# Optimization experiments

Measured on AMD Instinct MI355X. Metric: run time of the kernel, lower is better.

Reference implementation:

```python
import jax, jax.numpy as jnp
import numpy as np

N, E = 50000, 800000
IN_C, HID, HEADS, NUM_CLASSES = 256, 64, 4, 10
LRELU_SLOPE = 0.2
LN_EPS = 1e-5


def setup_inputs() -> dict:
    key = jax.random.key(0)
    ks = jax.random.split(key, 12)
    HC = HEADS * HID
    glorot = lambda k, shp: jax.random.normal(k, shp, jnp.float32) * np.sqrt(2.0 / (shp[0] + shp[-1]))
    return {
        "x": jax.random.normal(ks[0], (N, IN_C), jnp.float32),
        "edge_index": jax.random.randint(ks[1], (2, E), 0, N, jnp.int64),
        "edge_weight": jax.random.uniform(ks[2], (E, 1), jnp.float32),
        "W": glorot(ks[3], (IN_C, HC)),
        "att_src": glorot(ks[4], (1, HEADS, HID)),
        "att_dst": glorot(ks[5], (1, HEADS, HID)),
        "att_edge": glorot(ks[6], (1, HEADS, HID)),
        "W_edge": glorot(ks[7], (1, HC)),
        "bias": jnp.zeros((HC,), jnp.float32),
        "ln_gamma": jnp.ones((HC,), jnp.float32),
        "ln_beta": jnp.zeros((HC,), jnp.float32),
        "fc_W": glorot(ks[8], (HC, NUM_CLASSES)),
        "fc_b": jnp.zeros((NUM_CLASSES,), jnp.float32),
    }


def reference(x, edge_index, edge_weight, W, att_src, att_dst, att_edge,
              W_edge, bias, ln_gamma, ln_beta, fc_W, fc_b):
    n = x.shape[0]
    src, dst = edge_index[0], edge_index[1]

    # GATConv: linear projection -> [N, H, C]
    xh = (x @ W).reshape(n, HEADS, HID)
    a_src = jnp.sum(xh * att_src, axis=-1)  # [N, H]
    a_dst = jnp.sum(xh * att_dst, axis=-1)  # [N, H]

    # edge feature projection (edge_dim=1) -> per-edge attention term
    eh = (edge_weight @ W_edge).reshape(-1, HEADS, HID)  # [E, H, C]
    a_edge = jnp.sum(eh * att_edge, axis=-1)             # [E, H]

    alpha = a_src[src] + a_dst[dst] + a_edge             # [E, H]
    alpha = jax.nn.leaky_relu(alpha, LRELU_SLOPE)

    # segment softmax over incoming edges of each destination node
    amax = jax.ops.segment_max(alpha, dst, num_segments=n)  # [N, H]
    amax = jnp.where(jnp.isfinite(amax), amax, 0.0)
    ex = jnp.exp(alpha - amax[dst])
    esum = jax.ops.segment_sum(ex, dst, num_segments=n)     # [N, H]
    attn = ex / (esum[dst] + 1e-16)                          # [E, H]

    # message = gathered source features weighted by attention; scatter-add
    msg = xh[src] * attn[:, :, None]                          # [E, H, C]
    out = jax.ops.segment_sum(msg, dst, num_segments=n)      # [N, H, C]
    out = out.reshape(n, HEADS * HID) + bias                  # concat heads

    # LayerNorm + ReLU (dropout is identity in eval) + Linear head
    mu = jnp.mean(out, axis=-1, keepdims=True)
    var = jnp.mean(jnp.square(out - mu), axis=-1, keepdims=True)
    out = (out - mu) * jax.lax.rsqrt(var + LN_EPS) * ln_gamma + ln_beta
    out = jax.nn.relu(out)
    return out @ fc_W + fc_b
```

## Files before the change

kernel.cpp:

```cpp
#include <hip/hip_runtime.h>
#include <hip/hip_bf16.h>

static constexpr int HEADS = 4;
static constexpr int HID   = 64;
static constexpr int HC    = 256;
static constexpr int NCLS  = 10;

typedef short    bf16x8 __attribute__((ext_vector_type(8)));
typedef _Float16 f16x8  __attribute__((ext_vector_type(8)));
typedef _Float16 f16x4  __attribute__((ext_vector_type(4)));
typedef float    f32x4  __attribute__((ext_vector_type(4)));

__device__ inline unsigned short f2bf(float f) {
    union { float f; unsigned u; } c; c.f = f;
    unsigned r = (c.u + 0x7fff + ((c.u >> 16) & 1)) >> 16;
    return (unsigned short)r;
}
__device__ inline unsigned short f2h(float f) {
    _Float16 h = (_Float16)f; unsigned short u; __builtin_memcpy(&u, &h, 2); return u;
}
__device__ inline float h2f(unsigned short u) {
    _Float16 h; __builtin_memcpy(&h, &u, 2); return (float)h;
}

__global__ void prep_kernel(const float* __restrict__ We, const float* __restrict__ attE,
                            float* __restrict__ cE, const float* __restrict__ W,
                            unsigned short* __restrict__ Wt, const float* __restrict__ fcW,
                            unsigned short* __restrict__ fcWh) {
    int b = blockIdx.x, t = threadIdx.x;
    if (b == 0) {
        float p = We[t] * attE[t];
#pragma unroll
        for (int d = 32; d; d >>= 1) p += __shfl_xor(p, d, 64);
        if ((t & 63) == 0) cE[t >> 6] = p;
    } else if (b <= 256) {
        int k = b - 1;
        Wt[t * 256 + k] = f2bf(W[k * 256 + t]);
    } else {
        int j = b - 257;
        unsigned short v = 0;
        if (j < NCLS) v = f2h(fcW[t * NCLS + j]);
        fcWh[j * 256 + t] = v;
    }
}

__global__ __launch_bounds__(256) void gemm_mfma(const float* __restrict__ X,
                                                 const unsigned short* __restrict__ Bt,
                                                 unsigned short* __restrict__ XHh, int M) {
    __shared__ alignas(16) unsigned short As[128][40];
    __shared__ alignas(16) unsigned short Bs[128][40];
    const int tid = threadIdx.x;
    const int lane = tid & 63, wid = tid >> 6;
    const int wr = wid >> 1, wc = wid & 1;
    const int bm = blockIdx.x * 128, bn = blockIdx.y * 128;
    const int fr = lane & 15, kg = lane >> 4;

    f32x4 acc[4][4] = {};

    for (int k0 = 0; k0 < 256; k0 += 32) {
        __syncthreads();
#pragma unroll
        for (int ss = 0; ss < 4; ++ss) {
            int idx = tid + (ss << 8);
            int row = idx >> 3, seg = idx & 7;
            int grow = bm + row;
            float4 av = make_float4(0.f, 0.f, 0.f, 0.f);
            if (grow < M) av = *(const float4*)&X[(size_t)grow * 256 + k0 + seg * 4];
            ushort4 ab = make_ushort4(f2bf(av.x), f2bf(av.y), f2bf(av.z), f2bf(av.w));
            *(ushort4*)&As[row][seg * 4] = ab;
        }
#pragma unroll
        for (int qq = 0; qq < 2; ++qq) {
            int q = tid + (qq << 8);
            int row = q >> 2, part = q & 3;
            const ushort4* bp = (const ushort4*)&Bt[(size_t)(bn + row) * 256 + k0 + part * 8];
            *(ushort4*)&Bs[row][part * 8]     = bp[0];
            *(ushort4*)&Bs[row][part * 8 + 4] = bp[1];
        }
        __syncthreads();

        bf16x8 af[4], bf[4];
#pragma unroll
        for (int i = 0; i < 4; ++i)
            af[i] = *(const bf16x8*)&As[wr * 64 + i * 16 + fr][kg * 8];
#pragma unroll
        for (int j = 0; j < 4; ++j)
            bf[j] = *(const bf16x8*)&Bs[wc * 64 + j * 16 + fr][kg * 8];
#pragma unroll
        for (int i = 0; i < 4; ++i)
#pragma unroll
            for (int j = 0; j < 4; ++j)
                acc[i][j] = __builtin_amdgcn_mfma_f32_16x16x32_bf16(af[i], bf[j], acc[i][j], 0, 0, 0);
    }

#pragma unroll
    for (int i = 0; i < 4; ++i) {
#pragma unroll
        for (int j = 0; j < 4; ++j) {
            int col = bn + wc * 64 + j * 16 + fr;
#pragma unroll
            for (int r = 0; r < 4; ++r) {
                int row = bm + wr * 64 + i * 16 + kg * 4 + r;
                if (row < M) XHh[(size_t)row * 256 + col] = f2h(acc[i][j][r]);
            }
        }
    }
}

__global__ __launch_bounds__(256) void attn_coef(const unsigned short* __restrict__ xhh,
                                                 const float* __restrict__ attS,
                                                 const float* __restrict__ attD,
                                                 float* __restrict__ a_src,
                                                 float* __restrict__ a_dst,
                                                 int Nn) {
    int wid = threadIdx.x >> 6, lane = threadIdx.x & 63;
    int n = blockIdx.x * 4 + wid;
    if (n >= Nn) return;
    ushort4 xv = *(const ushort4*)&xhh[(size_t)n * HC + lane * 4];
    float x0 = h2f(xv.x), x1 = h2f(xv.y), x2 = h2f(xv.z), x3 = h2f(xv.w);
    float4 sv = *(const float4*)&attS[lane * 4];
    float4 dv = *(const float4*)&attD[lane * 4];
    float ps = x0 * sv.x + x1 * sv.y + x2 * sv.z + x3 * sv.w;
    float pd = x0 * dv.x + x1 * dv.y + x2 * dv.z + x3 * dv.w;
#pragma unroll
    for (int d = 1; d < 16; d <<= 1) {
        ps += __shfl_xor(ps, d, 64);
        pd += __shfl_xor(pd, d, 64);
    }
    if ((lane & 15) == 0) {
        a_src[n * 4 + (lane >> 4)] = ps;
        a_dst[n * 4 + (lane >> 4)] = pd;
    }
}

__global__ void hist_kernel(const int* __restrict__ dst, int* __restrict__ deg,
                            int* __restrict__ rank, int E) {
    int e = blockIdx.x * 256 + threadIdx.x;
    if (e < E) rank[e] = atomicAdd(&deg[dst[e]], 1);
}

__global__ __launch_bounds__(1024) void scan1(const int* __restrict__ deg,
                                              int* __restrict__ row_start,
                                              int* __restrict__ bsum, int n) {
    __shared__ int wsum[16];
    const int tid = threadIdx.x, lane = tid & 63, wid = tid >> 6;
    int i = blockIdx.x * 1024 + tid;
    int v = (i < n) ? ((deg[i] + 3) & ~3) : 0;
    int incl = v;
#pragma unroll
    for (int d = 1; d < 64; d <<= 1) {
        int t = __shfl_up(incl, d, 64);
        if (lane >= d) incl += t;
    }
    if (lane == 63) wsum[wid] = incl;
    __syncthreads();
    if (tid < 16) {
        int w = wsum[tid];
#pragma unroll
        for (int d = 1; d < 16; d <<= 1) {
            int t = __shfl_up(w, d, 16);
            if (tid >= d) w += t;
        }
        wsum[tid] = w;
    }
    __syncthreads();
    int waveoff = wid ? wsum[wid - 1] : 0;
    if (i < n) row_start[i] = waveoff + incl - v;
    if (tid == 1023) bsum[blockIdx.x] = waveoff + incl;
}

__global__ __launch_bounds__(1024) void scan23(int* __restrict__ row_start,
                                               const int* __restrict__ bsum, int n, int nb) {
    __shared__ int pref[64];
    const int tid = threadIdx.x;
    if (tid < 64) {
        int v = (tid < nb) ? bsum[tid] : 0;
#pragma unroll
        for (int d = 1; d < 64; d <<= 1) {
            int t = __shfl_up(v, d, 64);
            if (tid >= d) v += t;
        }
        pref[tid] = v;
    }
    __syncthreads();
    int add = blockIdx.x ? pref[blockIdx.x - 1] : 0;
    int i = blockIdx.x * 1024 + tid;
    if (i < n) row_start[i] += add;
    if (i == n) row_start[n] = pref[nb - 1];
}

__global__ void scatter_p(const int* __restrict__ src, const int* __restrict__ dst,
                          const float* __restrict__ ew, const float* __restrict__ a_src,
                          const float* __restrict__ a_dst, const float* __restrict__ cE,
                          const int* __restrict__ row_start, const int* __restrict__ rank,
                          int* __restrict__ srcs, float* __restrict__ pq, int E) {
    int e = blockIdx.x * 256 + threadIdx.x;
    if (e >= E) return;
    int s = src[e], d = dst[e];
    float w = ew[e];
    float4 as_ = *(const float4*)&a_src[s * 4];
    float4 ad_ = *(const float4*)&a_dst[d * 4];
    float4 ce  = *(const float4*)cE;
    int pos = row_start[d] + rank[e];
    srcs[pos] = s;
    float al[4] = {as_.x + ad_.x + ce.x * w, as_.y + ad_.y + ce.y * w,
                   as_.z + ad_.z + ce.z * w, as_.w + ad_.w + ce.w * w};
    float* base = pq + ((size_t)(pos >> 2)) * 16 + (pos & 3);
#pragma unroll
    for (int h = 0; h < 4; ++h) {
        float a = al[h] > 0.f ? al[h] : 0.2f * al[h];
        base[h * 4] = __expf(a);
    }
}

__global__ __launch_bounds__(256) void gat_main(
    const unsigned short* __restrict__ xhh, const int* __restrict__ row_start,
    const int* __restrict__ deg, const int* __restrict__ srcs,
    const float* __restrict__ pq, const float* __restrict__ bias,
    const float* __restrict__ gamma, const float* __restrict__ beta,
    unsigned short* __restrict__ yh, int Nn) {
    const int lane = threadIdx.x & 63, wid = threadIdx.x >> 6;
    const int n = blockIdx.x * 4 + wid;
    if (n >= Nn) return;
    const int myh = lane >> 4;
    const int rs = row_start[n];
    const int dn = deg[n];
    const int nfull = dn >> 2, rem = dn & 3;
    const unsigned short* xl = xhh + (size_t)lane * 4;

    f32x4 acc = {0.f, 0.f, 0.f, 0.f};
    float psum = 0.f;

#define LOADMETA(c, S, P)                                                     \
    S = *(const int4*)&srcs[rs + (c) * 4];                                    \
    P = *(const float4*)&pq[((size_t)((rs >> 2) + (c))) * 16 + myh * 4];
#define GATHER(S, X0, X1, X2, X3)                                             \
    X0 = *(const f16x4*)(xl + (size_t)__builtin_amdgcn_readfirstlane((S).x) * HC); \
    X1 = *(const f16x4*)(xl + (size_t)__builtin_amdgcn_readfirstlane((S).y) * HC); \
    X2 = *(const f16x4*)(xl + (size_t)__builtin_amdgcn_readfirstlane((S).z) * HC); \
    X3 = *(const f16x4*)(xl + (size_t)__builtin_amdgcn_readfirstlane((S).w) * HC);
#define COMPUTE(P, X0, X1, X2, X3)                                            \
    psum += ((P).x + (P).y) + ((P).z + (P).w);                                \
    acc[0] = fmaf((P).x, (float)(X0).x, acc[0]);                              \
    acc[1] = fmaf((P).x, (float)(X0).y, acc[1]);                              \
    acc[2] = fmaf((P).x, (float)(X0).z, acc[2]);                              \
    acc[3] = fmaf((P).x, (float)(X0).w, acc[3]);                              \
    acc[0] = fmaf((P).y, (float)(X1).x, acc[0]);                              \
    acc[1] = fmaf((P).y, (float)(X1).y, acc[1]);                              \
    acc[2] = fmaf((P).y, (float)(X1).z, acc[2]);                              \
    acc[3] = fmaf((P).y, (float)(X1).w, acc[3]);                              \
    acc[0] = fmaf((P).z, (float)(X2).x, acc[0]);                              \
    acc[1] = fmaf((P).z, (float)(X2).y, acc[1]);                              \
    acc[2] = fmaf((P).z, (float)(X2).z, acc[2]);                              \
    acc[3] = fmaf((P).z, (float)(X2).w, acc[3]);                              \
    acc[0] = fmaf((P).w, (float)(X3).x, acc[0]);                              \
    acc[1] = fmaf((P).w, (float)(X3).y, acc[1]);                              \
    acc[2] = fmaf((P).w, (float)(X3).z, acc[2]);                              \
    acc[3] = fmaf((P).w, (float)(X3).w, acc[3]);

    if (nfull > 0) {
        int4 s0, sN = {0, 0, 0, 0}, s2 = {0, 0, 0, 0};
        float4 pC, pN = {0.f, 0.f, 0.f, 0.f}, p2 = {0.f, 0.f, 0.f, 0.f};
        f16x4 g0, g1, g2, g3;
        LOADMETA(0, s0, pC);
        GATHER(s0, g0, g1, g2, g3);
        if (nfull > 1) { LOADMETA(1, sN, pN); }
        for (int c = 0; c < nfull; ++c) {
            f16x4 h0, h1, h2, h3;
            if (c + 1 < nfull) { GATHER(sN, h0, h1, h2, h3); }
            if (c + 2 < nfull) { LOADMETA(c + 2, s2, p2); }
            COMPUTE(pC, g0, g1, g2, g3);
            pC = pN; pN = p2; sN = s2;
            g0 = h0; g1 = h1; g2 = h2; g3 = h3;
        }
    }
    if (rem) {
        int4 s; float4 p;
        LOADMETA(nfull, s, p);
        p.w = 0.f;
        if (rem < 3) p.z = 0.f;
        if (rem < 2) p.y = 0.f;
        int b0 = __builtin_amdgcn_readfirstlane(s.x);
        int b1 = rem > 1 ? __builtin_amdgcn_readfirstlane(s.y) : b0;
        int b2 = rem > 2 ? __builtin_amdgcn_readfirstlane(s.z) : b0;
        f16x4 x0 = *(const f16x4*)(xl + (size_t)b0 * HC);
        f16x4 x1 = *(const f16x4*)(xl + (size_t)b1 * HC);
        f16x4 x2 = *(const f16x4*)(xl + (size_t)b2 * HC);
        COMPUTE(p, x0, x1, x2, x0);
    }
#undef LOADMETA
#undef GATHER
#undef COMPUTE

    float rin = 1.f / (psum + 1e-16f);

    float4 bv = *(const float4*)&bias[lane * 4];
    float v0 = acc[0] * rin + bv.x;
    float v1 = acc[1] * rin + bv.y;
    float v2 = acc[2] * rin + bv.z;
    float v3 = acc[3] * rin + bv.w;

    float s1 = v0 + v1 + v2 + v3;
    float s2v = v0 * v0 + v1 * v1 + v2 * v2 + v3 * v3;
#pragma unroll
    for (int d = 1; d < 64; d <<= 1) {
        s1 += __shfl_xor(s1, d, 64);
        s2v += __shfl_xor(s2v, d, 64);
    }
    float mu = s1 * (1.f / 256.f);
    float var = s2v * (1.f / 256.f) - mu * mu;
    float rstd = rsqrtf(var + 1e-5f);
    float4 gv = *(const float4*)&gamma[lane * 4];
    float4 btv = *(const float4*)&beta[lane * 4];
    float y0 = fmaxf((v0 - mu) * rstd * gv.x + btv.x, 0.f);
    float y1 = fmaxf((v1 - mu) * rstd * gv.y + btv.y, 0.f);
    float y2 = fmaxf((v2 - mu) * rstd * gv.z + btv.z, 0.f);
    float y3 = fmaxf((v3 - mu) * rstd * gv.w + btv.w, 0.f);

    f16x4 yv;
    yv.x = (_Float16)y0; yv.y = (_Float16)y1; yv.z = (_Float16)y2; yv.w = (_Float16)y3;
    *(f16x4*)&yh[(size_t)n * HC + lane * 4] = yv;
}

__global__ __launch_bounds__(256) void fc_gemm(const unsigned short* __restrict__ yh,
                                               const unsigned short* __restrict__ fcWh,
                                               const float* __restrict__ fcb,
                                               float* __restrict__ out, int M) {
    const int lane = threadIdx.x & 63, wid = threadIdx.x >> 6;
    const int rowbase = blockIdx.x * 256 + wid * 64;
    const int fr = lane & 15, kg = lane >> 4;
    f32x4 acc[4] = {};
#pragma unroll
    for (int k0 = 0; k0 < 256; k0 += 32) {
        f16x8 bfr = *(const f16x8*)&fcWh[fr * 256 + k0 + kg * 8];
#pragma unroll
        for (int i = 0; i < 4; ++i) {
            int row = rowbase + i * 16 + fr;
            f16x8 afr = {};
            if (row < M) afr = *(const f16x8*)&yh[(size_t)row * 256 + k0 + kg * 8];
            acc[i] = __builtin_amdgcn_mfma_f32_16x16x32_f16(afr, bfr, acc[i], 0, 0, 0);
        }
    }
    if (fr < NCLS) {
        float bb = fcb[fr];
#pragma unroll
        for (int i = 0; i < 4; ++i) {
#pragma unroll
            for (int r = 0; r < 4; ++r) {
                int row = rowbase + i * 16 + kg * 4 + r;
                if (row < M) out[(size_t)row * NCLS + fr] = acc[i][r] + bb;
            }
        }
    }
}

extern "C" void kernel_launch(void* const* d_in, const int* in_sizes, int n_in,
                              void* d_out, int out_size, void* d_ws, size_t ws_size,
                              hipStream_t stream) {
    const float* x    = (const float*)d_in[0];
    const int*   ei   = (const int*)d_in[1];
    const float* ew   = (const float*)d_in[2];
    const float* W    = (const float*)d_in[3];
    const float* attS = (const float*)d_in[4];
    const float* attD = (const float*)d_in[5];
    const float* attE = (const float*)d_in[6];
    const float* We   = (const float*)d_in[7];
    const float* bias = (const float*)d_in[8];
    const float* gam  = (const float*)d_in[9];
    const float* bet  = (const float*)d_in[10];
    const float* fcW  = (const float*)d_in[11];
    const float* fcb  = (const float*)d_in[12];
    float* out = (float*)d_out;

    const int Nn = in_sizes[0] / HC;
    const int E  = in_sizes[1] / 2;
    const int* src = ei;
    const int* dst = ei + E;
    const int nb = (Nn + 1023) / 1024;
    const int EpMax = E + 4 * Nn;

    char* ws = (char*)d_ws;
    size_t off = 0;
    auto alloc = [&](size_t bytes) { void* p = ws + off; off = (off + bytes + 255) & ~size_t(255); return p; };
    unsigned short* xhh  = (unsigned short*)alloc((size_t)Nn * HC * 2);
    unsigned short* yh   = (unsigned short*)alloc((size_t)Nn * HC * 2);
    unsigned short* wt   = (unsigned short*)alloc((size_t)HC * HC * 2);
    unsigned short* fcWh = (unsigned short*)alloc((size_t)16 * HC * 2);
    float* a_srcb    = (float*)alloc((size_t)Nn * 4 * 4);
    float* a_dstb    = (float*)alloc((size_t)Nn * 4 * 4);
    float* cE        = (float*)alloc(256);
    int*   row_start = (int*)  alloc((size_t)(Nn + 1) * 4);
    int*   deg       = (int*)  alloc((size_t)Nn * 4);
    int*   bsum      = (int*)  alloc((size_t)nb * 4);
    int*   rank      = (int*)  alloc((size_t)E * 4);
    int*   srcs      = (int*)  alloc((size_t)EpMax * 4);
    float* pq        = (float*)alloc((size_t)EpMax * 16);
    (void)ws_size;

    hipMemsetAsync(deg, 0, (size_t)Nn * 4, stream);

    prep_kernel<<<273, 256, 0, stream>>>(We, attE, cE, W, wt, fcW, fcWh);

    dim3 g((Nn + 127) / 128, 2);
    gemm_mfma<<<g, 256, 0, stream>>>(x, wt, xhh, Nn);

    attn_coef<<<(Nn + 3) / 4, 256, 0, stream>>>(xhh, attS, attD, a_srcb, a_dstb, Nn);
    hist_kernel<<<(E + 255) / 256, 256, 0, stream>>>(dst, deg, rank, E);
    scan1<<<nb, 1024, 0, stream>>>(deg, row_start, bsum, Nn);
    scan23<<<nb, 1024, 0, stream>>>(row_start, bsum, Nn, nb);
    scatter_p<<<(E + 255) / 256, 256, 0, stream>>>(src, dst, ew, a_srcb, a_dstb, cE,
                                                   row_start, rank, srcs, pq, E);
    gat_main<<<(Nn + 3) / 4, 256, 0, stream>>>(xhh, row_start, deg, srcs, pq,
                                               bias, gam, bet, yh, Nn);
    fc_gemm<<<(Nn + 255) / 256, 256, 0, stream>>>(yh, fcWh, fcb, out, Nn);
}
```

Measured before the change: 202.1 us.

## Use persistent work-queue GAT aggregation with zero-padded edge groups

The aggregation kernel becomes persistent: a fixed grid of 2048 blocks whose waves grab batches of four destination nodes from an atomic counter. The counter is reset inside the prep kernel. The scan kernel now zero-fills each node's padded edge slots in srcs and pq, so the main loop handles only whole groups of four edges, with no remainder branch. The gather loop is unrolled four deep with double-buffered feature loads. The goal is to balance skewed node degrees, overlap gathers with compute, and avoid per-node launch cost, at the price of atomic contention and extra padding writes.

```diff
diff --git a/kernel.cpp b/kernel.cpp
--- a/kernel.cpp
+++ b/kernel.cpp
@@ -26,9 +26,10 @@
 __global__ void prep_kernel(const float* __restrict__ We, const float* __restrict__ attE,
                             float* __restrict__ cE, const float* __restrict__ W,
                             unsigned short* __restrict__ Wt, const float* __restrict__ fcW,
-                            unsigned short* __restrict__ fcWh) {
+                            unsigned short* __restrict__ fcWh, int* __restrict__ qctr) {
     int b = blockIdx.x, t = threadIdx.x;
     if (b == 0) {
+        if (t == 0) qctr[0] = 0;
         float p = We[t] * attE[t];
 #pragma unroll
         for (int d = 32; d; d >>= 1) p += __shfl_xor(p, d, 64);
@@ -170,7 +171,10 @@
 }
 
 __global__ __launch_bounds__(1024) void scan23(int* __restrict__ row_start,
-                                               const int* __restrict__ bsum, int n, int nb) {
+                                               const int* __restrict__ bsum,
+                                               const int* __restrict__ deg,
+                                               int* __restrict__ srcs,
+                                               float* __restrict__ pq, int n, int nb) {
     __shared__ int pref[64];
     const int tid = threadIdx.x;
     if (tid < 64) {
@@ -185,7 +189,18 @@
     __syncthreads();
     int add = blockIdx.x ? pref[blockIdx.x - 1] : 0;
     int i = blockIdx.x * 1024 + tid;
-    if (i < n) row_start[i] += add;
+    if (i < n) {
+        int v = row_start[i] + add;
+        row_start[i] = v;
+        int dn = deg[i];
+        int pd = (dn + 3) & ~3;
+        for (int s = dn; s < pd; ++s) {
+            int pos = v + s;
+            srcs[pos] = 0;
+            float* b = pq + (size_t)(pos >> 2) * 16 + (pos & 3);
+            b[0] = 0.f; b[4] = 0.f; b[8] = 0.f; b[12] = 0.f;
+        }
+    }
     if (i == n) row_start[n] = pref[nb - 1];
 }
 
@@ -215,111 +230,124 @@
 
 __global__ __launch_bounds__(256) void gat_main(
     const unsigned short* __restrict__ xhh, const int* __restrict__ row_start,
-    const int* __restrict__ deg, const int* __restrict__ srcs,
-    const float* __restrict__ pq, const float* __restrict__ bias,
-    const float* __restrict__ gamma, const float* __restrict__ beta,
-    unsigned short* __restrict__ yh, int Nn) {
-    const int lane = threadIdx.x & 63, wid = threadIdx.x >> 6;
-    const int n = blockIdx.x * 4 + wid;
-    if (n >= Nn) return;
-    const int myh = lane >> 4;
-    const int rs = row_start[n];
-    const int dn = deg[n];
-    const int nfull = dn >> 2, rem = dn & 3;
-    const unsigned short* xl = xhh + (size_t)lane * 4;
-
-    f32x4 acc = {0.f, 0.f, 0.f, 0.f};
-    float psum = 0.f;
-
-#define LOADMETA(c, S, P)                                                     \
-    S = *(const int4*)&srcs[rs + (c) * 4];                                    \
-    P = *(const float4*)&pq[((size_t)((rs >> 2) + (c))) * 16 + myh * 4];
-#define GATHER(S, X0, X1, X2, X3)                                             \
-    X0 = *(const f16x4*)(xl + (size_t)__builtin_amdgcn_readfirstlane((S).x) * HC); \
-    X1 = *(const f16x4*)(xl + (size_t)__builtin_amdgcn_readfirstlane((S).y) * HC); \
-    X2 = *(const f16x4*)(xl + (size_t)__builtin_amdgcn_readfirstlane((S).z) * HC); \
-    X3 = *(const f16x4*)(xl + (size_t)__builtin_amdgcn_readfirstlane((S).w) * HC);
-#define COMPUTE(P, X0, X1, X2, X3)                                            \
-    psum += ((P).x + (P).y) + ((P).z + (P).w);                                \
-    acc[0] = fmaf((P).x, (float)(X0).x, acc[0]);                              \
-    acc[1] = fmaf((P).x, (float)(X0).y, acc[1]);                              \
-    acc[2] = fmaf((P).x, (float)(X0).z, acc[2]);                              \
-    acc[3] = fmaf((P).x, (float)(X0).w, acc[3]);                              \
-    acc[0] = fmaf((P).y, (float)(X1).x, acc[0]);                              \
-    acc[1] = fmaf((P).y, (float)(X1).y, acc[1]);                              \
-    acc[2] = fmaf((P).y, (float)(X1).z, acc[2]);                              \
-    acc[3] = fmaf((P).y, (float)(X1).w, acc[3]);                              \
-    acc[0] = fmaf((P).z, (float)(X2).x, acc[0]);                              \
-    acc[1] = fmaf((P).z, (float)(X2).y, acc[1]);                              \
-    acc[2] = fmaf((P).z, (float)(X2).z, acc[2]);                              \
-    acc[3] = fmaf((P).z, (float)(X2).w, acc[3]);                              \
-    acc[0] = fmaf((P).w, (float)(X3).x, acc[0]);                              \
-    acc[1] = fmaf((P).w, (float)(X3).y, acc[1]);                              \
-    acc[2] = fmaf((P).w, (float)(X3).z, acc[2]);                              \
-    acc[3] = fmaf((P).w, (float)(X3).w, acc[3]);
-
-    if (nfull > 0) {
-        int4 s0, sN = {0, 0, 0, 0}, s2 = {0, 0, 0, 0};
-        float4 pC, pN = {0.f, 0.f, 0.f, 0.f}, p2 = {0.f, 0.f, 0.f, 0.f};
-        f16x4 g0, g1, g2, g3;
-        LOADMETA(0, s0, pC);
-        GATHER(s0, g0, g1, g2, g3);
-        if (nfull > 1) { LOADMETA(1, sN, pN); }
-        for (int c = 0; c < nfull; ++c) {
-            f16x4 h0, h1, h2, h3;
-            if (c + 1 < nfull) { GATHER(sN, h0, h1, h2, h3); }
-            if (c + 2 < nfull) { LOADMETA(c + 2, s2, p2); }
-            COMPUTE(pC, g0, g1, g2, g3);
-            pC = pN; pN = p2; sN = s2;
-            g0 = h0; g1 = h1; g2 = h2; g3 = h3;
-        }
-    }
-    if (rem) {
-        int4 s; float4 p;
-        LOADMETA(nfull, s, p);
-        p.w = 0.f;
-        if (rem < 3) p.z = 0.f;
-        if (rem < 2) p.y = 0.f;
-        int b0 = __builtin_amdgcn_readfirstlane(s.x);
-        int b1 = rem > 1 ? __builtin_amdgcn_readfirstlane(s.y) : b0;
-        int b2 = rem > 2 ? __builtin_amdgcn_readfirstlane(s.z) : b0;
-        f16x4 x0 = *(const f16x4*)(xl + (size_t)b0 * HC);
-        f16x4 x1 = *(const f16x4*)(xl + (size_t)b1 * HC);
-        f16x4 x2 = *(const f16x4*)(xl + (size_t)b2 * HC);
-        COMPUTE(p, x0, x1, x2, x0);
-    }
-#undef LOADMETA
-#undef GATHER
-#undef COMPUTE
-
-    float rin = 1.f / (psum + 1e-16f);
-
-    float4 bv = *(const float4*)&bias[lane * 4];
-    float v0 = acc[0] * rin + bv.x;
-    float v1 = acc[1] * rin + bv.y;
-    float v2 = acc[2] * rin + bv.z;
-    float v3 = acc[3] * rin + bv.w;
-
-    float s1 = v0 + v1 + v2 + v3;
-    float s2v = v0 * v0 + v1 * v1 + v2 * v2 + v3 * v3;
-#pragma unroll
-    for (int d = 1; d < 64; d <<= 1) {
-        s1 += __shfl_xor(s1, d, 64);
-        s2v += __shfl_xor(s2v, d, 64);
-    }
-    float mu = s1 * (1.f / 256.f);
-    float var = s2v * (1.f / 256.f) - mu * mu;
-    float rstd = rsqrtf(var + 1e-5f);
-    float4 gv = *(const float4*)&gamma[lane * 4];
-    float4 btv = *(const float4*)&beta[lane * 4];
-    float y0 = fmaxf((v0 - mu) * rstd * gv.x + btv.x, 0.f);
-    float y1 = fmaxf((v1 - mu) * rstd * gv.y + btv.y, 0.f);
-    float y2 = fmaxf((v2 - mu) * rstd * gv.z + btv.z, 0.f);
-    float y3 = fmaxf((v3 - mu) * rstd * gv.w + btv.w, 0.f);
-
-    f16x4 yv;
-    yv.x = (_Float16)y0; yv.y = (_Float16)y1; yv.z = (_Float16)y2; yv.w = (_Float16)y3;
-    *(f16x4*)&yh[(size_t)n * HC + lane * 4] = yv;
+    const int* __restrict__ srcs, const float* __restrict__ pq,
+    const float* __restrict__ bias, const float* __restrict__ gamma,
+    const float* __restrict__ beta, unsigned short* __restrict__ yh,
+    int* __restrict__ qctr, int Nn) {
+    const int lane = threadIdx.x & 63;
+    const int myh4 = (lane >> 4) << 2;
+
+    const float4 bv  = *(const float4*)&bias[lane * 4];
+    const float4 gv  = *(const float4*)&gamma[lane * 4];
+    const float4 btv = *(const float4*)&beta[lane * 4];
+
+#define META(S, P, c_) do {                                                    \
+    S = *(const int4*)(srcs + (size_t)(rs4 + (c_)) * 4);                       \
+    P = *(const float4*)(pq + (size_t)(rs4 + (c_)) * 16 + myh4);               \
+} while (0)
+#define GAT1(A, t_) do {                                                       \
+    int t = (t_);                                                              \
+    if ((unsigned)t >= (unsigned)Nn) t = 0;                                    \
+    A = ((const f16x4*)(xhh + (size_t)t * HC))[lane];                          \
+} while (0)
+#define GATH(A0, A1, A2, A3, S) do {                                           \
+    GAT1(A0, (S).x); GAT1(A1, (S).y); GAT1(A2, (S).z); GAT1(A3, (S).w);        \
+} while (0)
+#define COMP(P, A0, A1, A2, A3) do {                                           \
+    psum += ((P).x + (P).y) + ((P).z + (P).w);                                 \
+    acc[0] = fmaf((P).x, (float)(A0).x, acc[0]);                               \
+    acc[1] = fmaf((P).x, (float)(A0).y, acc[1]);                               \
+    acc[2] = fmaf((P).x, (float)(A0).z, acc[2]);                               \
+    acc[3] = fmaf((P).x, (float)(A0).w, acc[3]);                               \
+    acc[0] = fmaf((P).y, (float)(A1).x, acc[0]);                               \
+    acc[1] = fmaf((P).y, (float)(A1).y, acc[1]);                               \
+    acc[2] = fmaf((P).y, (float)(A1).z, acc[2]);                               \
+    acc[3] = fmaf((P).y, (float)(A1).w, acc[3]);                               \
+    acc[0] = fmaf((P).z, (float)(A2).x, acc[0]);                               \
+    acc[1] = fmaf((P).z, (float)(A2).y, acc[1]);                               \
+    acc[2] = fmaf((P).z, (float)(A2).z, acc[2]);                               \
+    acc[3] = fmaf((P).z, (float)(A2).w, acc[3]);                               \
+    acc[0] = fmaf((P).w, (float)(A3).x, acc[0]);                               \
+    acc[1] = fmaf((P).w, (float)(A3).y, acc[1]);                               \
+    acc[2] = fmaf((P).w, (float)(A3).z, acc[2]);                               \
+    acc[3] = fmaf((P).w, (float)(A3).w, acc[3]);                               \
+} while (0)
+
+    for (;;) {
+        int pop0 = 0;
+        if (lane == 0) pop0 = atomicAdd(qctr, 4);
+        int nb_ = __builtin_amdgcn_readfirstlane(pop0);
+        if (nb_ >= Nn) break;
+        int nend = (nb_ + 4 < Nn) ? nb_ + 4 : Nn;
+
+        for (int n = nb_; n < nend; ++n) {
+            const int rs = row_start[n], re = row_start[n + 1];
+            const int rs4 = rs >> 2;
+            const int G = (re - rs) >> 2;
+
+            f32x4 acc = {0.f, 0.f, 0.f, 0.f};
+            float psum = 0.f;
+
+            if (G > 0) {
+                int4 s0, s1, s2, s3;
+                float4 p0, p1, p2, p3;
+                f16x4 A0, A1, A2, A3, B0, B1, B2, B3;
+                META(s0, p0, 0); META(s1, p1, 1); META(s2, p2, 2); META(s3, p3, 3);
+                GATH(A0, A1, A2, A3, s0);
+                int c = 0;
+                for (; c + 4 <= G; c += 4) {
+                    GATH(B0, B1, B2, B3, s1); COMP(p0, A0, A1, A2, A3); META(s0, p0, c + 4);
+                    GATH(A0, A1, A2, A3, s2); COMP(p1, B0, B1, B2, B3); META(s1, p1, c + 5);
+                    GATH(B0, B1, B2, B3, s3); COMP(p2, A0, A1, A2, A3); META(s2, p2, c + 6);
+                    GATH(A0, A1, A2, A3, s0); COMP(p3, B0, B1, B2, B3); META(s3, p3, c + 7);
+                }
+                int k = G - c;
+                if (k == 1) {
+                    COMP(p0, A0, A1, A2, A3);
+                } else if (k == 2) {
+                    GATH(B0, B1, B2, B3, s1);
+                    COMP(p0, A0, A1, A2, A3);
+                    COMP(p1, B0, B1, B2, B3);
+                } else if (k == 3) {
+                    GATH(B0, B1, B2, B3, s1);
+                    COMP(p0, A0, A1, A2, A3);
+                    GATH(A0, A1, A2, A3, s2);
+                    COMP(p1, B0, B1, B2, B3);
+                    COMP(p2, A0, A1, A2, A3);
+                }
+            }
+
+            float rin = 1.f / (psum + 1e-16f);
+            float v0 = acc[0] * rin + bv.x;
+            float v1 = acc[1] * rin + bv.y;
+            float v2 = acc[2] * rin + bv.z;
+            float v3 = acc[3] * rin + bv.w;
+
+            float s1r = v0 + v1 + v2 + v3;
+            float s2r = v0 * v0 + v1 * v1 + v2 * v2 + v3 * v3;
+#pragma unroll
+            for (int d = 1; d < 64; d <<= 1) {
+                s1r += __shfl_xor(s1r, d, 64);
+                s2r += __shfl_xor(s2r, d, 64);
+            }
+            float mu = s1r * (1.f / 256.f);
+            float var = s2r * (1.f / 256.f) - mu * mu;
+            float rstd = rsqrtf(var + 1e-5f);
+            float y0 = fmaxf((v0 - mu) * rstd * gv.x + btv.x, 0.f);
+            float y1 = fmaxf((v1 - mu) * rstd * gv.y + btv.y, 0.f);
+            float y2 = fmaxf((v2 - mu) * rstd * gv.z + btv.z, 0.f);
+            float y3 = fmaxf((v3 - mu) * rstd * gv.w + btv.w, 0.f);
+
+            f16x4 yv;
+            yv.x = (_Float16)y0; yv.y = (_Float16)y1;
+            yv.z = (_Float16)y2; yv.w = (_Float16)y3;
+            *(f16x4*)&yh[(size_t)n * HC + lane * 4] = yv;
+        }
+    }
+#undef META
+#undef GAT1
+#undef GATH
+#undef COMP
 }
 
 __global__ __launch_bounds__(256) void fc_gemm(const unsigned short* __restrict__ yh,
@@ -389,17 +417,18 @@
     float* a_srcb    = (float*)alloc((size_t)Nn * 4 * 4);
     float* a_dstb    = (float*)alloc((size_t)Nn * 4 * 4);
     float* cE        = (float*)alloc(256);
+    int*   qctr      = (int*)  alloc(256);
     int*   row_start = (int*)  alloc((size_t)(Nn + 1) * 4);
     int*   deg       = (int*)  alloc((size_t)Nn * 4);
     int*   bsum      = (int*)  alloc((size_t)nb * 4);
     int*   rank      = (int*)  alloc((size_t)E * 4);
-    int*   srcs      = (int*)  alloc((size_t)EpMax * 4);
-    float* pq        = (float*)alloc((size_t)EpMax * 16);
+    int*   srcs      = (int*)  alloc((size_t)EpMax * 4 + 256);
+    float* pq        = (float*)alloc((size_t)EpMax * 16 + 1024);
     (void)ws_size;
 
     hipMemsetAsync(deg, 0, (size_t)Nn * 4, stream);
 
-    prep_kernel<<<273, 256, 0, stream>>>(We, attE, cE, W, wt, fcW, fcWh);
+    prep_kernel<<<273, 256, 0, stream>>>(We, attE, cE, W, wt, fcW, fcWh, qctr);
 
     dim3 g((Nn + 127) / 128, 2);
     gemm_mfma<<<g, 256, 0, stream>>>(x, wt, xhh, Nn);
@@ -407,10 +436,10 @@
     attn_coef<<<(Nn + 3) / 4, 256, 0, stream>>>(xhh, attS, attD, a_srcb, a_dstb, Nn);
     hist_kernel<<<(E + 255) / 256, 256, 0, stream>>>(dst, deg, rank, E);
     scan1<<<nb, 1024, 0, stream>>>(deg, row_start, bsum, Nn);
-    scan23<<<nb, 1024, 0, stream>>>(row_start, bsum, Nn, nb);
+    scan23<<<nb, 1024, 0, stream>>>(row_start, bsum, deg, srcs, pq, Nn, nb);
     scatter_p<<<(E + 255) / 256, 256, 0, stream>>>(src, dst, ew, a_srcb, a_dstb, cE,
                                                    row_start, rank, srcs, pq, E);
-    gat_main<<<(Nn + 3) / 4, 256, 0, stream>>>(xhh, row_start, deg, srcs, pq,
-                                               bias, gam, bet, yh, Nn);
+    gat_main<<<2048, 256, 0, stream>>>(xhh, row_start, srcs, pq,
+                                       bias, gam, bet, yh, qctr, Nn);
     fc_gemm<<<(Nn + 255) / 256, 256, 0, stream>>>(yh, fcWh, fcb, out, Nn);
 }
```

Measured after the change: 401.3 us. 98.6% more time.

## Split edge scatter from attention-score computation into a per-node pass

Applied to the files above, without the earlier changes.

The per-edge scatter kernel now writes only the source index and edge weight into CSR order. A new per-destination-node kernel computes the leaky-ReLU exponentials from these sorted arrays and writes pq with coalesced stores, including explicit zeros for padding slots. The scan kernel also zero-fills the padded srcs slots. The aim is to replace scattered random 16-byte pq writes and per-edge a_dst gathers with more regular accesses. The cost is an extra kernel launch plus an extra write and read of the sorted source and weight arrays.

```diff
diff --git a/kernel.cpp b/kernel.cpp
--- a/kernel.cpp
+++ b/kernel.cpp
@@ -170,7 +170,9 @@
 }
 
 __global__ __launch_bounds__(1024) void scan23(int* __restrict__ row_start,
-                                               const int* __restrict__ bsum, int n, int nb) {
+                                               const int* __restrict__ bsum,
+                                               const int* __restrict__ deg,
+                                               int* __restrict__ srcs, int n, int nb) {
     __shared__ int pref[64];
     const int tid = threadIdx.x;
     if (tid < 64) {
@@ -185,31 +187,52 @@
     __syncthreads();
     int add = blockIdx.x ? pref[blockIdx.x - 1] : 0;
     int i = blockIdx.x * 1024 + tid;
-    if (i < n) row_start[i] += add;
+    if (i < n) {
+        int v = row_start[i] + add;
+        row_start[i] = v;
+        int dn = deg[i];
+        int pd = (dn + 3) & ~3;
+        for (int s = dn; s < pd; ++s) srcs[v + s] = 0;
+    }
     if (i == n) row_start[n] = pref[nb - 1];
 }
 
-__global__ void scatter_p(const int* __restrict__ src, const int* __restrict__ dst,
-                          const float* __restrict__ ew, const float* __restrict__ a_src,
-                          const float* __restrict__ a_dst, const float* __restrict__ cE,
-                          const int* __restrict__ row_start, const int* __restrict__ rank,
-                          int* __restrict__ srcs, float* __restrict__ pq, int E) {
+__global__ void scatter_sw(const int* __restrict__ src, const int* __restrict__ dst,
+                           const float* __restrict__ ew,
+                           const int* __restrict__ row_start, const int* __restrict__ rank,
+                           int* __restrict__ srcs, float* __restrict__ ews, int E) {
     int e = blockIdx.x * 256 + threadIdx.x;
     if (e >= E) return;
-    int s = src[e], d = dst[e];
-    float w = ew[e];
-    float4 as_ = *(const float4*)&a_src[s * 4];
-    float4 ad_ = *(const float4*)&a_dst[d * 4];
-    float4 ce  = *(const float4*)cE;
-    int pos = row_start[d] + rank[e];
-    srcs[pos] = s;
-    float al[4] = {as_.x + ad_.x + ce.x * w, as_.y + ad_.y + ce.y * w,
-                   as_.z + ad_.z + ce.z * w, as_.w + ad_.w + ce.w * w};
-    float* base = pq + ((size_t)(pos >> 2)) * 16 + (pos & 3);
-#pragma unroll
-    for (int h = 0; h < 4; ++h) {
-        float a = al[h] > 0.f ? al[h] : 0.2f * al[h];
-        base[h * 4] = __expf(a);
+    int pos = row_start[dst[e]] + rank[e];
+    srcs[pos] = src[e];
+    ews[pos] = ew[e];
+}
+
+__global__ __launch_bounds__(256) void p_pass(
+    const int* __restrict__ row_start, const int* __restrict__ deg,
+    const int* __restrict__ srcs, const float* __restrict__ ews,
+    const float* __restrict__ a_src, const float* __restrict__ a_dst,
+    const float* __restrict__ cE, float* __restrict__ pq, int Nn) {
+    const int wid = threadIdx.x >> 6, lane = threadIdx.x & 63;
+    const int n = blockIdx.x * 4 + wid;
+    if (n >= Nn) return;
+    const int rs = row_start[n];
+    const int dn = deg[n];
+    const int pd = (dn + 3) & ~3;
+    const int slot0 = lane >> 2, h = lane & 3;
+    const float adn = a_dst[n * 4 + h];
+    const float ceh = cE[h];
+    for (int s = slot0; s < pd; s += 16) {
+        int pos = rs + s;
+        float p = 0.f;
+        if (s < dn) {
+            int sv = srcs[pos];
+            float w = ews[pos];
+            float a = a_src[sv * 4 + h] + adn + ceh * w;
+            a = fmaxf(a, 0.2f * a);
+            p = __expf(a);
+        }
+        pq[(size_t)(pos >> 2) * 16 + h * 4 + (pos & 3)] = p;
     }
 }
 
@@ -393,8 +416,9 @@
     int*   deg       = (int*)  alloc((size_t)Nn * 4);
     int*   bsum      = (int*)  alloc((size_t)nb * 4);
     int*   rank      = (int*)  alloc((size_t)E * 4);
-    int*   srcs      = (int*)  alloc((size_t)EpMax * 4);
-    float* pq        = (float*)alloc((size_t)EpMax * 16);
+    int*   srcs      = (int*)  alloc((size_t)EpMax * 4 + 256);
+    float* ews       = (float*)alloc((size_t)EpMax * 4 + 256);
+    float* pq        = (float*)alloc((size_t)EpMax * 16 + 1024);
     (void)ws_size;
 
     hipMemsetAsync(deg, 0, (size_t)Nn * 4, stream);
@@ -407,9 +431,11 @@
     attn_coef<<<(Nn + 3) / 4, 256, 0, stream>>>(xhh, attS, attD, a_srcb, a_dstb, Nn);
     hist_kernel<<<(E + 255) / 256, 256, 0, stream>>>(dst, deg, rank, E);
     scan1<<<nb, 1024, 0, stream>>>(deg, row_start, bsum, Nn);
-    scan23<<<nb, 1024, 0, stream>>>(row_start, bsum, Nn, nb);
-    scatter_p<<<(E + 255) / 256, 256, 0, stream>>>(src, dst, ew, a_srcb, a_dstb, cE,
-                                                   row_start, rank, srcs, pq, E);
+    scan23<<<nb, 1024, 0, stream>>>(row_start, bsum, deg, srcs, Nn, nb);
+    scatter_sw<<<(E + 255) / 256, 256, 0, stream>>>(src, dst, ew, row_start, rank,
+                                                    srcs, ews, E);
+    p_pass<<<(Nn + 3) / 4, 256, 0, stream>>>(row_start, deg, srcs, ews,
+                                             a_srcb, a_dstb, cE, pq, Nn);
     gat_main<<<(Nn + 3) / 4, 256, 0, stream>>>(xhh, row_start, deg, srcs, pq,
                                                bias, gam, bet, yh, Nn);
     fc_gemm<<<(Nn + 255) / 256, 256, 0, stream>>>(yh, fcWh, fcb, out, Nn);
```

Result: slower. 208.0 us (+2.9%).
